# Kernel optimization log

Hardware: AMD Instinct MI355X
Metric: run time of the kernel (lower is better)

Reference implementation:

```python
import jax, jax.numpy as jnp
import numpy as np
from jax import lax

K_SIZE = 5  # dilated_kernel_size


def dcls_kernel(w, p, k=K_SIZE):
    """Build dense (Cout,Cin,k,k) kernel from DCLS v1 bilinear interpolation.
    w: (Cout,Cin,Kc) weights; p: (2,Cout,Cin,Kc) learnable positions."""
    lim = k // 2
    pos = jnp.clip(p, -lim, lim) + lim          # in [0, k-1]
    i = jnp.floor(pos).astype(jnp.int32)
    r = pos - i                                  # bilinear fractions
    Co, Ci, Kc = w.shape
    co = jnp.arange(Co)[:, None, None]
    ci = jnp.arange(Ci)[None, :, None]
    i1, i2 = i[0], i[1]
    r1, r2 = r[0], r[1]
    # scatter into (k+1)x(k+1) grid so i+1 never goes out of bounds, then trim
    K = jnp.zeros((Co, Ci, k + 1, k + 1), w.dtype)
    K = K.at[co, ci, i1,     i2    ].add(w * (1 - r1) * (1 - r2))
    K = K.at[co, ci, i1 + 1, i2    ].add(w * r1 * (1 - r2))
    K = K.at[co, ci, i1,     i2 + 1].add(w * (1 - r1) * r2)
    K = K.at[co, ci, i1 + 1, i2 + 1].add(w * r1 * r2)
    return K[:, :, :k, :k]


def conv2d(x, K, pad):
    return lax.conv_general_dilated(
        x, K, window_strides=(1, 1), padding=[(pad, pad), (pad, pad)],
        dimension_numbers=('NCHW', 'OIHW', 'NCHW'))


def maxpool2(x):
    return lax.reduce_window(x, -jnp.inf, lax.max, (1, 1, 2, 2), (1, 1, 2, 2), 'VALID')


def setup_inputs() -> dict:
    key = jax.random.key(0)
    ks = jax.random.split(key, 12)
    lim = K_SIZE // 2
    B = 4096
    x = jax.random.normal(ks[0], (B, 1, 28, 28), jnp.float32)
    w1 = jax.random.normal(ks[1], (32, 1, 16), jnp.float32) * 0.2
    p1 = jax.random.uniform(ks[2], (2, 32, 1, 16), jnp.float32, -lim, lim)
    b1 = jnp.zeros((32,), jnp.float32)
    w2 = jax.random.normal(ks[3], (64, 32, 32), jnp.float32) * 0.05
    p2 = jax.random.uniform(ks[4], (2, 64, 32, 32), jnp.float32, -lim, lim)
    b2 = jnp.zeros((64,), jnp.float32)
    fc1_w = jax.random.normal(ks[5], (128, 64 * 7 * 7), jnp.float32) * 0.02
    fc1_b = jnp.zeros((128,), jnp.float32)
    fc2_w = jax.random.normal(ks[6], (10, 128), jnp.float32) * 0.08
    fc2_b = jnp.zeros((10,), jnp.float32)
    return dict(x=x, w1=w1, p1=p1, b1=b1, w2=w2, p2=p2, b2=b2,
                fc1_w=fc1_w, fc1_b=fc1_b, fc2_w=fc2_w, fc2_b=fc2_b)


def reference(x, w1, p1, b1, w2, p2, b2, fc1_w, fc1_b, fc2_w, fc2_b):
    h = conv2d(x, dcls_kernel(w1, p1), pad=2) + b1[None, :, None, None]
    h = maxpool2(jax.nn.relu(h))                       # (B,32,14,14)
    h = conv2d(h, dcls_kernel(w2, p2), pad=2) + b2[None, :, None, None]
    h = maxpool2(jax.nn.relu(h))                       # (B,64,7,7)
    h = h.reshape(-1, 64 * 7 * 7)
    h = jax.nn.relu(h @ fc1_w.T + fc1_b)
    return h @ fc2_w.T + fc2_b                         # (B,10)
```

## Files before the change

### kernel.cpp

```cpp
#include <hip/hip_runtime.h>
#include <hip/hip_bf16.h>

typedef __attribute__((ext_vector_type(8))) short short8;
typedef __attribute__((ext_vector_type(4))) short short4v;
typedef __attribute__((ext_vector_type(4))) float float4v;
typedef __attribute__((ext_vector_type(16))) float float16v;

static __device__ __forceinline__ unsigned short f2bf(float f) {
    unsigned u = __float_as_uint(f);
    unsigned r = (u + 0x7FFF + ((u >> 16) & 1)) >> 16;
    return (unsigned short)r;
}

__global__ __launch_bounds__(256) void prep_all(
    const float* __restrict__ w1, const float* __restrict__ p1,
    const float* __restrict__ w2, const float* __restrict__ p2,
    const float* __restrict__ fc1w,
    unsigned short* __restrict__ K1b,
    unsigned short* __restrict__ Kt,
    unsigned short* __restrict__ w1b) {
    const int blk = blockIdx.x;
    const int t = threadIdx.x;

    if (blk < 8) {
        int cell = blk * 256 + t;
        int co = cell >> 6;
        int k = cell & 63;
        int wr = k >> 3;
        int kx = k & 7;
        float acc = 0.f;
        if (wr < 5 && kx < 5) {
#pragma unroll 8
            for (int kc = 0; kc < 16; ++kc) {
                float wv = w1[co * 16 + kc];
                float pa = p1[co * 16 + kc];
                float pb = p1[512 + co * 16 + kc];
                float pos1 = fminf(fmaxf(pa, -2.f), 2.f) + 2.f;
                float pos2 = fminf(fmaxf(pb, -2.f), 2.f) + 2.f;
                int i1 = (int)floorf(pos1);
                int i2 = (int)floorf(pos2);
                float r1 = pos1 - (float)i1;
                float r2 = pos2 - (float)i2;
                float c = 0.f;
                if (i1 == wr && i2 == kx) c += (1.f - r1) * (1.f - r2);
                if (i1 + 1 == wr && i2 == kx) c += r1 * (1.f - r2);
                if (i1 == wr && i2 + 1 == kx) c += (1.f - r1) * r2;
                if (i1 + 1 == wr && i2 + 1 == kx) c += r1 * r2;
                acc += wv * c;
            }
        }
        K1b[cell] = f2bf(acc);
    } else if (blk < 208) {
        int cell = (blk - 8) * 256 + t;
        int kk = cell >> 11;
        int co = (cell >> 5) & 63;
        int ci = cell & 31;
        int ky = kk / 5;
        int kx = kk - 5 * ky;
        const int base = (co * 32 + ci) * 32;
        float acc = 0.f;
#pragma unroll 8
        for (int kc = 0; kc < 32; ++kc) {
            float wv = w2[base + kc];
            float pa = p2[base + kc];
            float pb = p2[65536 + base + kc];
            float pos1 = fminf(fmaxf(pa, -2.f), 2.f) + 2.f;
            float pos2 = fminf(fmaxf(pb, -2.f), 2.f) + 2.f;
            int i1 = (int)floorf(pos1);
            int i2 = (int)floorf(pos2);
            float r1 = pos1 - (float)i1;
            float r2 = pos2 - (float)i2;
            float c = 0.f;
            if (i1 == ky && i2 == kx) c += (1.f - r1) * (1.f - r2);
            if (i1 + 1 == ky && i2 == kx) c += r1 * (1.f - r2);
            if (i1 == ky && i2 + 1 == kx) c += (1.f - r1) * r2;
            if (i1 + 1 == ky && i2 + 1 == kx) c += r1 * r2;
            acc += wv * c;
        }
        int nt = co >> 5, mq = co & 31;
        int kh2 = ci >> 4, hh = (ci >> 3) & 1, jj = ci & 7;
        Kt[kk * 2048 + nt * 1024 + kh2 * 512 + hh * 256 + mq * 8 + jj] = f2bf(acc);
    } else {
        int i8 = ((blk - 208) * 256 + t) * 8;
        float4 v0 = *(const float4*)(fc1w + i8);
        float4 v1 = *(const float4*)(fc1w + i8 + 4);
        short8 o = {(short)f2bf(v0.x), (short)f2bf(v0.y), (short)f2bf(v0.z),
                    (short)f2bf(v0.w), (short)f2bf(v1.x), (short)f2bf(v1.y),
                    (short)f2bf(v1.z), (short)f2bf(v1.w)};
        *(short8*)(w1b + i8) = o;
    }
}

__global__ __launch_bounds__(256, 3) void fused_conv_mfma(
    const float* __restrict__ x,
    const unsigned short* __restrict__ K1b,
    const unsigned short* __restrict__ Kt,
    const float* __restrict__ b1,
    const float* __restrict__ b2,
    unsigned short* __restrict__ h2) {
    __shared__ __align__(16) unsigned short h1p[18 * 20 * 40];
    __shared__ __align__(16) unsigned short sm4[4 * 29 * 44];
    __shared__ __align__(16) unsigned short sm_xb[784];

    const int b = blockIdx.x;
    const int tid = threadIdx.x;
    const int lane = tid & 63;
    const int wv = tid >> 6;
    const int n16 = lane & 15;
    const int cig = lane >> 4;

    const int yi = 2 * (n16 >> 3) + ((n16 >> 1) & 1);
    const int xi = 2 * ((n16 >> 2) & 1) + (n16 & 1);
    const int pYo = cig >> 1, pXo = cig & 1;

    const int mq = lane & 31;
    const int Qx = mq >> 2;
    const int dy2 = (mq >> 1) & 1;
    const int dx2 = mq & 1;
    const int hh = lane >> 5;

    for (int t = tid; t < 1800; t += 256) ((uint4*)h1p)[t] = uint4{0, 0, 0, 0};
    {
        const float* xb = x + (size_t)b * 784;
        for (int t = tid; t < 784; t += 256) sm_xb[t] = f2bf(xb[t]);
    }
    __syncthreads();

    if (tid < 116) {
        int s = tid / 29;
        int r = tid - s * 29;
        unsigned short* dst = sm4 + (s * 29 + r) * 44;
        bool rok = r < 28;
#pragma unroll
        for (int g2 = 0; g2 < 11; ++g2) {
            short4v v;
#pragma unroll
            for (int e = 0; e < 4; ++e) {
                int c = g2 * 4 + e + s - 4;
                v[e] = (short)((rok && (unsigned)c < 28u) ? sm_xb[r * 28 + c]
                                                          : (unsigned short)0);
            }
            *(short4v*)(dst + g2 * 4) = v;
        }
    }

    short8 bw[2][2];
    float bias1[2], bias2n[2];
#pragma unroll
    for (int cot = 0; cot < 2; ++cot) {
#pragma unroll
        for (int h = 0; h < 2; ++h)
            bw[cot][h] = *(const short8*)(K1b + (cot * 16 + n16) * 64 + h * 32 + cig * 8);
        bias1[cot] = b1[cot * 16 + n16];
    }
#pragma unroll
    for (int nt = 0; nt < 2; ++nt) bias2n[nt] = b2[nt * 32 + mq];

    const int s1 = (xi + 2) & 3;
    const int pb1 = (xi + 2) & ~3;
    const unsigned short* a1base = sm4 + s1 * (29 * 44) + pb1;

    __syncthreads();

    for (int i = 0; i < 13; ++i) {
        int t = wv + 4 * i;
        if (t < 49) {
            int tY = t / 7, tX = t - 7 * tY;
            const unsigned short* ab = a1base + 4 * tX;
            int r0 = 4 * tY + yi - 2 + cig;
            int r1 = r0 + 4;
            int rr0 = ((unsigned)r0 < 28u) ? r0 : 28;
            int rr1 = ((unsigned)r1 < 28u) ? r1 : 28;
            short4v lo0 = *(const short4v*)(ab + rr0 * 44);
            short4v hi0 = *(const short4v*)(ab + rr0 * 44 + 4);
            short4v lo1 = *(const short4v*)(ab + rr1 * 44);
            short4v hi1 = *(const short4v*)(ab + rr1 * 44 + 4);
            short8 af0 = {lo0[0], lo0[1], lo0[2], lo0[3], hi0[0], hi0[1], hi0[2], hi0[3]};
            short8 af1 = {lo1[0], lo1[1], lo1[2], lo1[3], hi1[0], hi1[1], hi1[2], hi1[3]};
            int pY = 2 * tY + pYo, pX = 2 * tX + pXo;
#pragma unroll
            for (int cot = 0; cot < 2; ++cot) {
                float4v acc = {0.f, 0.f, 0.f, 0.f};
                acc = __builtin_amdgcn_mfma_f32_16x16x32_bf16(af0, bw[cot][0], acc, 0, 0, 0);
                acc = __builtin_amdgcn_mfma_f32_16x16x32_bf16(af1, bw[cot][1], acc, 0, 0, 0);
                float v = fmaxf(fmaxf(acc[0], acc[1]), fmaxf(acc[2], acc[3]));
                v = fmaxf(v + bias1[cot], 0.f);
                h1p[((pY + 2) * 20 + (pX + 2)) * 40 + cot * 16 + n16] = f2bf(v);
            }
        }
    }

    int x2 = 2 * Qx + dx2;
    if (x2 > 13) x2 = 13;
    int aoff[2][2];
    int pYv[2];
#pragma unroll
    for (int mt = 0; mt < 2; ++mt) {
        int pY = 2 * wv + mt;
        int y2 = 2 * pY + dy2;
        if (y2 > 13) y2 = 13;
        pYv[mt] = pY;
#pragma unroll
        for (int kh2 = 0; kh2 < 2; ++kh2)
            aoff[mt][kh2] = (y2 * 20 + x2) * 40 + kh2 * 16 + hh * 8;
    }

    float16v acc2[2][2];
#pragma unroll
    for (int mt = 0; mt < 2; ++mt)
#pragma unroll
        for (int nt = 0; nt < 2; ++nt)
#pragma unroll
            for (int e = 0; e < 16; ++e) acc2[mt][nt][e] = 0.f;

    const unsigned short* KtL = Kt + lane * 8;

    short8 wfp[2][2][2];
#pragma unroll
    for (int nt = 0; nt < 2; ++nt)
#pragma unroll
        for (int q = 0; q < 2; ++q)
            wfp[0][nt][q] = *(const short8*)(KtL + nt * 1024 + q * 512);

    __syncthreads();

#pragma unroll
    for (int kk = 0; kk < 25; ++kk) {
        const int cs = kk & 1;
        const int ns = cs ^ 1;
        if (kk < 24) {
#pragma unroll
            for (int nt = 0; nt < 2; ++nt)
#pragma unroll
                for (int q = 0; q < 2; ++q)
                    wfp[ns][nt][q] = *(const short8*)(KtL + (kk + 1) * 2048 +
                                                      nt * 1024 + q * 512);
        }
        const int ky = kk / 5;
        const int kx = kk - 5 * ky;
        const int soff = (ky * 20 + kx) * 40;
        short8 aff[2][2];
#pragma unroll
        for (int mt = 0; mt < 2; ++mt)
#pragma unroll
            for (int q = 0; q < 2; ++q)
                aff[mt][q] = *(const short8*)(h1p + aoff[mt][q] + soff);

        __builtin_amdgcn_sched_barrier(0);
        __builtin_amdgcn_s_setprio(1);
#pragma unroll
        for (int mt = 0; mt < 2; ++mt)
#pragma unroll
            for (int nt = 0; nt < 2; ++nt) {
                acc2[mt][nt] = __builtin_amdgcn_mfma_f32_32x32x16_bf16(
                    aff[mt][0], wfp[cs][nt][0], acc2[mt][nt], 0, 0, 0);
                acc2[mt][nt] = __builtin_amdgcn_mfma_f32_32x32x16_bf16(
                    aff[mt][1], wfp[cs][nt][1], acc2[mt][nt], 0, 0, 0);
            }
        __builtin_amdgcn_s_setprio(0);
        __builtin_amdgcn_sched_barrier(0);
    }

    unsigned short* outb = h2 + (size_t)b * 3136;
#pragma unroll
    for (int mt = 0; mt < 2; ++mt) {
        if (pYv[mt] < 7) {
#pragma unroll
            for (int nt = 0; nt < 2; ++nt) {
#pragma unroll
                for (int g2 = 0; g2 < 4; ++g2) {
                    int pX = 2 * g2 + hh;
                    float v = fmaxf(fmaxf(acc2[mt][nt][4 * g2], acc2[mt][nt][4 * g2 + 1]),
                                    fmaxf(acc2[mt][nt][4 * g2 + 2], acc2[mt][nt][4 * g2 + 3]));
                    v = fmaxf(v + bias2n[nt], 0.f);
                    if (pX < 7)
                        outb[(nt * 32 + mq) * 49 + pYv[mt] * 7 + pX] = f2bf(v);
                }
            }
        }
    }
}

__global__ __launch_bounds__(256) void fc1_mfma(
    const unsigned short* __restrict__ A,
    const unsigned short* __restrict__ Wb,
    float* __restrict__ part, size_t PB) {
    __shared__ __align__(16) unsigned short As[64 * 72];
    const int blk = blockIdx.x;
    const int kh = blk % 7;
    const int m0 = (blk / 7) * 64;
    const int tid = threadIdx.x;
    const int wv = tid >> 6;
    const int lane = tid & 63;
    const int n16 = lane & 15;
    const int cig = lane >> 4;

    float4v acc[4][2];
#pragma unroll
    for (int mt = 0; mt < 4; ++mt)
#pragma unroll
        for (int j = 0; j < 2; ++j) acc[mt][j] = float4v{0.f, 0.f, 0.f, 0.f};

    for (int it = 0; it < 7; ++it) {
        int k0 = kh * 448 + it * 64;
        __syncthreads();
#pragma unroll
        for (int i = 0; i < 2; ++i) {
            int p = tid + 256 * i;
            int r = p >> 3, ko = (p & 7) * 8;
            *(short8*)(As + r * 72 + ko) =
                *(const short8*)(A + (size_t)(m0 + r) * 3136 + k0 + ko);
        }
        __syncthreads();
#pragma unroll
        for (int h = 0; h < 2; ++h) {
            short8 af[4];
#pragma unroll
            for (int mt = 0; mt < 4; ++mt)
                af[mt] = *(const short8*)(As + (mt * 16 + n16) * 72 + h * 32 + cig * 8);
            short8 wf[2];
#pragma unroll
            for (int j = 0; j < 2; ++j)
                wf[j] = *(const short8*)(Wb + (size_t)((wv * 2 + j) * 16 + n16) * 3136 +
                                         k0 + h * 32 + cig * 8);
#pragma unroll
            for (int mt = 0; mt < 4; ++mt)
#pragma unroll
                for (int j = 0; j < 2; ++j)
                    acc[mt][j] = __builtin_amdgcn_mfma_f32_16x16x32_bf16(
                        af[mt], wf[j], acc[mt][j], 0, 0, 0);
        }
    }
    float* o = part + (size_t)kh * PB;
#pragma unroll
    for (int mt = 0; mt < 4; ++mt)
#pragma unroll
        for (int j = 0; j < 2; ++j)
#pragma unroll
            for (int r = 0; r < 4; ++r) {
                int row = m0 + mt * 16 + cig * 4 + r;
                o[(size_t)row * 128 + (wv * 2 + j) * 16 + n16] = acc[mt][j][r];
            }
}

__global__ __launch_bounds__(256) void fc2_kernel(
    const float* __restrict__ part, size_t PB,
    const float* __restrict__ fc1b,
    const float* __restrict__ W, const float* __restrict__ bias,
    float* __restrict__ out) {
    __shared__ float smW[10 * 132];
    __shared__ float smB1[128];
    __shared__ float smB[10];
    int t = threadIdx.x;
    for (int i = t; i < 1280; i += 256) {
        int n = i >> 7, k = i & 127;
        smW[n * 132 + k] = W[i];
    }
    if (t < 128) smB1[t] = fc1b[t];
    if (t < 10) smB[t] = bias[t];
    __syncthreads();
    const int r = t >> 3;
    const int q = t & 7;
    const size_t b = (size_t)blockIdx.x * 32 + r;
    const float* pb = part + b * 128 + q * 16;

    float rv[16];
#pragma unroll
    for (int c = 0; c < 4; ++c) {
        float4 s = *(const float4*)(pb + 4 * c);
#pragma unroll
        for (int j = 1; j < 7; ++j) {
            float4 pj = *(const float4*)(pb + (size_t)j * PB + 4 * c);
            s.x += pj.x; s.y += pj.y; s.z += pj.z; s.w += pj.w;
        }
        float4 bv = *(const float4*)(smB1 + q * 16 + 4 * c);
        rv[4 * c + 0] = fmaxf(s.x + bv.x, 0.f);
        rv[4 * c + 1] = fmaxf(s.y + bv.y, 0.f);
        rv[4 * c + 2] = fmaxf(s.z + bv.z, 0.f);
        rv[4 * c + 3] = fmaxf(s.w + bv.w, 0.f);
    }
    float acc[10];
#pragma unroll
    for (int n = 0; n < 10; ++n) {
        const float4* wr = (const float4*)(smW + n * 132 + q * 16);
        float a = 0.f;
#pragma unroll
        for (int c = 0; c < 4; ++c) {
            float4 w = wr[c];
            a += rv[4 * c] * w.x + rv[4 * c + 1] * w.y +
                 rv[4 * c + 2] * w.z + rv[4 * c + 3] * w.w;
        }
        acc[n] = a;
    }
#pragma unroll
    for (int n = 0; n < 10; ++n) {
        acc[n] += __shfl_xor(acc[n], 1);
        acc[n] += __shfl_xor(acc[n], 2);
        acc[n] += __shfl_xor(acc[n], 4);
    }
    if (q == 0) {
#pragma unroll
        for (int n = 0; n < 10; ++n) out[b * 10 + n] = acc[n] + smB[n];
    }
}

extern "C" void kernel_launch(void* const* d_in, const int* in_sizes, int n_in,
                              void* d_out, int out_size, void* d_ws, size_t ws_size,
                              hipStream_t stream) {
    const float* x    = (const float*)d_in[0];
    const float* w1   = (const float*)d_in[1];
    const float* p1   = (const float*)d_in[2];
    const float* b1   = (const float*)d_in[3];
    const float* w2   = (const float*)d_in[4];
    const float* p2   = (const float*)d_in[5];
    const float* b2   = (const float*)d_in[6];
    const float* fc1w = (const float*)d_in[7];
    const float* fc1b = (const float*)d_in[8];
    const float* fc2w = (const float*)d_in[9];
    const float* fc2b = (const float*)d_in[10];
    float* out = (float*)d_out;

    const int B = in_sizes[0] / 784;

    float* ws = (float*)d_ws;
    unsigned short* Kt  = (unsigned short*)ws;
    unsigned short* K1b = (unsigned short*)(ws + 25600);
    unsigned short* w1b = (unsigned short*)(ws + 26624);
    unsigned short* h2b = (unsigned short*)(ws + 227328);
    float* fc1p = ws + 227328 + (size_t)B * 1568;

    prep_all<<<404, 256, 0, stream>>>(w1, p1, w2, p2, fc1w, K1b, Kt, w1b);
    fused_conv_mfma<<<B, 256, 0, stream>>>(x, K1b, Kt, b1, b2, h2b);
    fc1_mfma<<<(B / 64) * 7, 256, 0, stream>>>(h2b, w1b, fc1p, (size_t)B * 128);
    fc2_kernel<<<B / 32, 256, 0, stream>>>(fc1p, (size_t)B * 128,
                                           fc1b, fc2w, fc2b, out);
}
```

Baseline: 208.1 us.

## Split fused conv kernel into separate conv1 and conv2 kernels via global buffer

```diff
diff --git a/kernel.cpp b/kernel.cpp
--- a/kernel.cpp
+++ b/kernel.cpp
@@ -91,14 +91,11 @@
     }
 }
 
-__global__ __launch_bounds__(256, 3) void fused_conv_mfma(
+__global__ __launch_bounds__(256, 6) void conv1_mfma(
     const float* __restrict__ x,
     const unsigned short* __restrict__ K1b,
-    const unsigned short* __restrict__ Kt,
     const float* __restrict__ b1,
-    const float* __restrict__ b2,
-    unsigned short* __restrict__ h2) {
-    __shared__ __align__(16) unsigned short h1p[18 * 20 * 40];
+    unsigned short* __restrict__ h1g) {
     __shared__ __align__(16) unsigned short sm4[4 * 29 * 44];
     __shared__ __align__(16) unsigned short sm_xb[784];
 
@@ -113,13 +110,6 @@
     const int xi = 2 * ((n16 >> 2) & 1) + (n16 & 1);
     const int pYo = cig >> 1, pXo = cig & 1;
 
-    const int mq = lane & 31;
-    const int Qx = mq >> 2;
-    const int dy2 = (mq >> 1) & 1;
-    const int dx2 = mq & 1;
-    const int hh = lane >> 5;
-
-    for (int t = tid; t < 1800; t += 256) ((uint4*)h1p)[t] = uint4{0, 0, 0, 0};
     {
         const float* xb = x + (size_t)b * 784;
         for (int t = tid; t < 784; t += 256) sm_xb[t] = f2bf(xb[t]);
@@ -145,7 +135,7 @@
     }
 
     short8 bw[2][2];
-    float bias1[2], bias2n[2];
+    float bias1[2];
 #pragma unroll
     for (int cot = 0; cot < 2; ++cot) {
 #pragma unroll
@@ -153,8 +143,6 @@
             bw[cot][h] = *(const short8*)(K1b + (cot * 16 + n16) * 64 + h * 32 + cig * 8);
         bias1[cot] = b1[cot * 16 + n16];
     }
-#pragma unroll
-    for (int nt = 0; nt < 2; ++nt) bias2n[nt] = b2[nt * 32 + mq];
 
     const int s1 = (xi + 2) & 3;
     const int pb1 = (xi + 2) & ~3;
@@ -162,6 +150,7 @@
 
     __syncthreads();
 
+    unsigned short* outg = h1g + (size_t)b * 6272;
     for (int i = 0; i < 13; ++i) {
         int t = wv + 4 * i;
         if (t < 49) {
@@ -185,10 +174,33 @@
                 acc = __builtin_amdgcn_mfma_f32_16x16x32_bf16(af1, bw[cot][1], acc, 0, 0, 0);
                 float v = fmaxf(fmaxf(acc[0], acc[1]), fmaxf(acc[2], acc[3]));
                 v = fmaxf(v + bias1[cot], 0.f);
-                h1p[((pY + 2) * 20 + (pX + 2)) * 40 + cot * 16 + n16] = f2bf(v);
-            }
-        }
-    }
+                outg[(pY * 14 + pX) * 32 + cot * 16 + n16] = f2bf(v);
+            }
+        }
+    }
+}
+
+__global__ __launch_bounds__(256, 4) void conv2_mfma(
+    const unsigned short* __restrict__ h1g,
+    const unsigned short* __restrict__ Kt,
+    const float* __restrict__ b2,
+    unsigned short* __restrict__ h2) {
+    __shared__ __align__(16) unsigned short h1p[18 * 20 * 40];
+
+    const int b = blockIdx.x;
+    const int tid = threadIdx.x;
+    const int lane = tid & 63;
+    const int wv = tid >> 6;
+
+    const int mq = lane & 31;
+    const int Qx = mq >> 2;
+    const int dy2 = (mq >> 1) & 1;
+    const int dx2 = mq & 1;
+    const int hh = lane >> 5;
+
+    float bias2n[2];
+#pragma unroll
+    for (int nt = 0; nt < 2; ++nt) bias2n[nt] = b2[nt * 32 + mq];
 
     int x2 = 2 * Qx + dx2;
     if (x2 > 13) x2 = 13;
@@ -205,22 +217,35 @@
             aoff[mt][kh2] = (y2 * 20 + x2) * 40 + kh2 * 16 + hh * 8;
     }
 
-    float16v acc2[2][2];
-#pragma unroll
-    for (int mt = 0; mt < 2; ++mt)
-#pragma unroll
-        for (int nt = 0; nt < 2; ++nt)
-#pragma unroll
-            for (int e = 0; e < 16; ++e) acc2[mt][nt][e] = 0.f;
-
     const unsigned short* KtL = Kt + lane * 8;
-
     short8 wfp[2][2][2];
 #pragma unroll
     for (int nt = 0; nt < 2; ++nt)
 #pragma unroll
         for (int q = 0; q < 2; ++q)
             wfp[0][nt][q] = *(const short8*)(KtL + nt * 1024 + q * 512);
+
+    for (int t = tid; t < 1800; t += 256) ((uint4*)h1p)[t] = uint4{0, 0, 0, 0};
+    __syncthreads();
+    {
+        const unsigned short* src = h1g + (size_t)b * 6272;
+        for (int g = tid; g < 784; g += 256) {
+            int y = g / 56;
+            int r = g - y * 56;
+            int xx = r >> 2;
+            int q8 = r & 3;
+            *(short8*)(h1p + ((y + 2) * 20 + (xx + 2)) * 40 + q8 * 8) =
+                *(const short8*)(src + g * 8);
+        }
+    }
+
+    float16v acc2[2][2];
+#pragma unroll
+    for (int mt = 0; mt < 2; ++mt)
+#pragma unroll
+        for (int nt = 0; nt < 2; ++nt)
+#pragma unroll
+            for (int e = 0; e < 16; ++e) acc2[mt][nt][e] = 0.f;
 
     __syncthreads();
 
@@ -428,9 +453,11 @@
     unsigned short* w1b = (unsigned short*)(ws + 26624);
     unsigned short* h2b = (unsigned short*)(ws + 227328);
     float* fc1p = ws + 227328 + (size_t)B * 1568;
+    unsigned short* h1g = (unsigned short*)(ws + 227328 + (size_t)B * 2464);
 
     prep_all<<<404, 256, 0, stream>>>(w1, p1, w2, p2, fc1w, K1b, Kt, w1b);
-    fused_conv_mfma<<<B, 256, 0, stream>>>(x, K1b, Kt, b1, b2, h2b);
+    conv1_mfma<<<B, 256, 0, stream>>>(x, K1b, b1, h1g);
+    conv2_mfma<<<B, 256, 0, stream>>>(h1g, Kt, b2, h2b);
     fc1_mfma<<<(B / 64) * 7, 256, 0, stream>>>(h2b, w1b, fc1p, (size_t)B * 128);
     fc2_kernel<<<B / 32, 256, 0, stream>>>(fc1p, (size_t)B * 128,
                                            fc1b, fc2w, fc2b, out);
```

After: 223.8 us. 1.08x slower.
